# Kernel tuning notes

Measured on AMD Instinct MI355X. Metric: run time of the kernel, lower is better.

Reference implementation:

```python
import jax, jax.numpy as jnp
import numpy as np

B, T, NA, H, C = 64, 128, 2048, 1024, 10  # batch, time, n_act, hidden_units, classes
FORGET_BIAS = 1.0  # tf BasicLSTMCell default


def setup_inputs() -> dict:
    key = jax.random.key(0)
    ks = jax.random.split(key, 5)
    s = 0.02
    return {
        "inputs": jax.random.normal(ks[0], (B, T, NA), jnp.float32),
        "W0": jax.random.normal(ks[1], (NA + H, 4 * H), jnp.float32) * s,
        "b0": jnp.zeros((4 * H,), jnp.float32),
        "W1": jax.random.normal(ks[2], (2 * H, 4 * H), jnp.float32) * s,
        "b1": jnp.zeros((4 * H,), jnp.float32),
        "Wout": jax.random.normal(ks[3], (H, C), jnp.float32) * s,
        "bout": jnp.zeros((C,), jnp.float32),
    }


def _lstm_step(c, h, x, W, b):
    # tf.contrib.rnn.BasicLSTMCell: z = [x; h] @ W + b, gates order i, j, f, o
    z = jnp.concatenate([x, h], axis=-1) @ W + b
    i, j, f, o = jnp.split(z, 4, axis=-1)
    c_new = c * jax.nn.sigmoid(f + FORGET_BIAS) + jax.nn.sigmoid(i) * jnp.tanh(j)
    h_new = jnp.tanh(c_new) * jax.nn.sigmoid(o)
    return c_new, h_new


def reference(inputs, W0, b0, W1, b1, Wout, bout):
    Bz = inputs.shape[0]
    Hd = Wout.shape[0]

    def step(carry, x_t):
        c0, h0, c1, h1 = carry
        c0, h0 = _lstm_step(c0, h0, x_t, W0, b0)   # layer 0
        c1, h1 = _lstm_step(c1, h1, h0, W1, b1)    # layer 1
        return (c0, h0, c1, h1), h1

    z = jnp.zeros((Bz, Hd), inputs.dtype)
    init = (z, z, z, z)  # zero_state for both layers
    xs = jnp.swapaxes(inputs, 0, 1)  # [T, B, NA]
    _, hs = jax.lax.scan(step, init, xs)  # hs: [T, B, H]
    hs = jnp.swapaxes(hs, 0, 1)  # [B, T, H]
    logits = hs @ Wout + bout  # xw_plus_b on flattened outputs
    preds = jax.nn.softmax(logits, axis=-1)  # [B, T, C]
    return preds
```

## Files before the change

### kernel.cpp

```cpp
#include <hip/hip_runtime.h>
#include <stdint.h>


typedef __attribute__((ext_vector_type(4))) float f32x4;
typedef __attribute__((ext_vector_type(8))) short short8x;
typedef unsigned short ushort_t;

constexpr int B_  = 64;
constexpr int T_  = 128;
constexpr int NA_ = 2048;
constexpr int H_  = 1024;
constexpr int C_  = 10;
constexpr int BT_ = B_ * T_;
constexpr int G4_ = 4 * H_;
constexpr int HB_ = B_ * H_;
constexpr int CH_ = 32;
constexpr int MC_ = B_ * CH_;
constexpr int NWG_ = 256;

__device__ __forceinline__ ushort_t f2bf(float x) {
    uint32_t u = __float_as_uint(x);
    uint32_t r = (u + 0x7FFFu + ((u >> 16) & 1u)) >> 16;
    return (ushort_t)r;
}
__device__ __forceinline__ float bf2f(ushort_t h) {
    return __uint_as_float((uint32_t)h << 16);
}
__device__ __forceinline__ float sigmf(float x) { return 1.0f / (1.0f + expf(-x)); }

__device__ __forceinline__ void st_u32(void* p, uint32_t v) {
    __hip_atomic_store((uint32_t*)p, v, __ATOMIC_RELAXED, __HIP_MEMORY_SCOPE_AGENT);
}

#define AH_ISSUE(dst, ptr) \
    asm volatile("global_load_dwordx4 %0, %1, off sc0 sc1" : "=v"(dst) : "v"(ptr))

#define GLOAD_LDS(gp, lp) \
    __builtin_amdgcn_global_load_lds((const __attribute__((address_space(1))) uint32_t*)(gp), \
                                     (__attribute__((address_space(3))) uint32_t*)(lp), 16, 0, 0)

__global__ void decomp_chunk(const float* __restrict__ X, int c,
                             ushort_t* __restrict__ Hi, ushort_t* __restrict__ Lo) {
    const int i = blockIdx.x * blockDim.x + threadIdx.x;
    if (i >= MC_ * NA_ / 4) return;
    const int mp = i >> 9;
    const int kq = i & 511;
    const int b = mp >> 5, j = mp & 31;
    const size_t src = ((size_t)(b * T_ + c * CH_ + j)) * NA_ + (size_t)kq * 4;
    float4 v = *(const float4*)(X + src);
    ushort4 hi, lo;
    hi.x = f2bf(v.x); lo.x = f2bf(v.x - bf2f(hi.x));
    hi.y = f2bf(v.y); lo.y = f2bf(v.y - bf2f(hi.y));
    hi.z = f2bf(v.z); lo.z = f2bf(v.z - bf2f(hi.z));
    hi.w = f2bf(v.w); lo.w = f2bf(v.w - bf2f(hi.w));
    ((ushort4*)Hi)[i] = hi;
    ((ushort4*)Lo)[i] = lo;
}

__global__ void transdec(const float* __restrict__ W, int rowOff, int Klen,
                         ushort_t* __restrict__ Thi, ushort_t* __restrict__ Tlo,
                         int swz) {
    __shared__ float tile[32][33];
    const int k0 = blockIdx.x * 32, n0 = blockIdx.y * 32;
    const int tx = threadIdx.x & 31, ty = threadIdx.x >> 5;
#pragma unroll
    for (int i = 0; i < 32; i += 8)
        tile[ty + i][tx] = W[(size_t)(rowOff + k0 + ty + i) * G4_ + n0 + tx];
    __syncthreads();
#pragma unroll
    for (int i = 0; i < 32; i += 8) {
        float v = tile[tx][ty + i];
        int n = n0 + ty + i;
        int kk = k0 + tx;
        ushort_t hi = f2bf(v);
        Thi[(size_t)n * Klen + kk] = hi;
        int kl = swz ? (kk ^ ((n & 7) << 3)) : kk;
        Tlo[(size_t)n * Klen + kl] = f2bf(v - bf2f(hi));
    }
}

__global__ __launch_bounds__(256, 2)
void gemm_bf16x3(const ushort_t* __restrict__ Ahi, const ushort_t* __restrict__ Alo,
                 const ushort_t* __restrict__ Bhi, const ushort_t* __restrict__ Blo,
                 float* __restrict__ C, int M, int N, int K) {
    __shared__ ushort_t sA[2][128 * 64];
    __shared__ ushort_t sB[2][128 * 64];

    const int tid  = threadIdx.x;
    const int lane = tid & 63;
    const int wv   = tid >> 6;
    const int wr   = wv >> 1, wc = wv & 1;
    const int tiles_n = N >> 7;
    int id = blockIdx.x;
    const int q8 = gridDim.x >> 3;
    id = (id & 7) * q8 + (id >> 3);
    const int tm = (id / tiles_n) * 128, tn = (id % tiles_n) * 128;

    f32x4 acc[4][4] = {};

    for (int k0 = 0; k0 < K; k0 += 64) {
#pragma unroll
        for (int rd = 0; rd < 4; ++rd) {
            const int off = rd * 4096 + tid * 16;
            const int r   = off >> 7;
            const int kc  = ((off >> 4) & 7) ^ (r & 7);
            const size_t aoff = (size_t)(tm + r) * K + k0 + kc * 8;
            const size_t boff = (size_t)(tn + r) * K + k0 + kc * 8;
            const int dst = (rd * 4096 + wv * 1024) >> 1;
            GLOAD_LDS(Ahi + aoff, (ushort_t*)sA[0] + dst);
            GLOAD_LDS(Alo + aoff, (ushort_t*)sA[1] + dst);
            GLOAD_LDS(Bhi + boff, (ushort_t*)sB[0] + dst);
            GLOAD_LDS(Blo + boff, (ushort_t*)sB[1] + dst);
        }
        __syncthreads();
#pragma unroll
        for (int ks = 0; ks < 2; ++ks) {
            short8x ah[4], al[4], bh[4], bl[4];
#pragma unroll
            for (int i = 0; i < 4; ++i) {
                const int kc = ks * 4 + (lane >> 4);
                const int ra = wr * 64 + i * 16 + (lane & 15);
                const int ea = ra * 64 + ((kc ^ (ra & 7)) * 8);
                ah[i] = *(const short8x*)(&sA[0][ea]);
                al[i] = *(const short8x*)(&sA[1][ea]);
                const int rb = wc * 64 + i * 16 + (lane & 15);
                const int eb = rb * 64 + ((kc ^ (rb & 7)) * 8);
                bh[i] = *(const short8x*)(&sB[0][eb]);
                bl[i] = *(const short8x*)(&sB[1][eb]);
            }
#pragma unroll
            for (int i = 0; i < 4; ++i)
#pragma unroll
                for (int j = 0; j < 4; ++j) {
                    acc[i][j] = __builtin_amdgcn_mfma_f32_16x16x32_bf16(ah[i], bh[j], acc[i][j], 0, 0, 0);
                    acc[i][j] = __builtin_amdgcn_mfma_f32_16x16x32_bf16(ah[i], bl[j], acc[i][j], 0, 0, 0);
                    acc[i][j] = __builtin_amdgcn_mfma_f32_16x16x32_bf16(al[i], bh[j], acc[i][j], 0, 0, 0);
                }
        }
        __syncthreads();
    }
#pragma unroll
    for (int i = 0; i < 4; ++i)
#pragma unroll
        for (int j = 0; j < 4; ++j)
#pragma unroll
            for (int qq = 0; qq < 4; ++qq) {
                const int row = tm + wr * 64 + i * 16 + (lane >> 4) * 4 + qq;
                const int col = tn + wc * 64 + j * 16 + (lane & 15);
                C[(size_t)row * N + col] = acc[i][j][qq];
            }
}

__device__ __forceinline__ void grid_bar(unsigned* slots, unsigned* flag, unsigned epoch) {
    __syncthreads();
    if (threadIdx.x == 0)
        __hip_atomic_store(&slots[blockIdx.x], epoch, __ATOMIC_RELAXED, __HIP_MEMORY_SCOPE_AGENT);
    if (blockIdx.x == 0) {
        if (threadIdx.x < NWG_) {
            unsigned spins = 0;
            while (__hip_atomic_load(&slots[threadIdx.x], __ATOMIC_RELAXED, __HIP_MEMORY_SCOPE_AGENT) < epoch
                   && ++spins < (1u << 20))
                __builtin_amdgcn_s_sleep(4);
        }
        __syncthreads();
        if (threadIdx.x == 0)
            __hip_atomic_store(flag, epoch, __ATOMIC_RELAXED, __HIP_MEMORY_SCOPE_AGENT);
    } else {
        if (threadIdx.x == 0) {
            unsigned spins = 0;
            while (__hip_atomic_load(flag, __ATOMIC_RELAXED, __HIP_MEMORY_SCOPE_AGENT) < epoch
                   && ++spins < (1u << 20))
                __builtin_amdgcn_s_sleep(4);
        }
    }
    __syncthreads();
}

__global__ __launch_bounds__(512, 1)
void lstm_persist(int t0, int t1,
                  const float* __restrict__ Z0c,
                  const ushort_t* __restrict__ W0hT_hi, const ushort_t* __restrict__ W0hT_lo,
                  const ushort_t* __restrict__ W1T_hi,  const ushort_t* __restrict__ W1T_lo,
                  const float* __restrict__ b0, const float* __restrict__ b1,
                  ushort_t* __restrict__ h0blk, ushort_t* __restrict__ h1blk,
                  float* __restrict__ c0, float* __restrict__ c1,
                  ushort_t* __restrict__ hsblk, unsigned* slots, unsigned* flag) {
    const int w = blockIdx.x;
    const bool isL0 = (w < 128);
    const int uB = isL0 ? w : (w - 128);
    const int u0 = uB * 8;
    const int tid = threadIdx.x, lane = tid & 63, kv = tid >> 6;
    const int K   = isL0 ? H_ : 2 * H_;
    const int KS  = K >> 3;
    const int NKS = KS >> 5;
    const int kbase = kv * KS;

    __shared__ ushort_t slo[32 * 2048];
    __shared__ float zbuf[64][33];

    const ushort_t* Whi = isL0 ? W0hT_hi : W1T_hi;
    const ushort_t* Wlo = isL0 ? W0hT_lo : W1T_lo;

    const int nis = K >> 9;
    for (int g = 0; g < 4; ++g)
        for (int is = 0; is < nis; ++is) {
            const size_t selem = (size_t)(g * H_ + u0) * K + is * 4096 + kv * 512 + (size_t)lane * 8;
            ushort_t* dst = slo + g * 8 * K + is * 4096 + kv * 512;
            GLOAD_LDS(Wlo + selem, dst);
        }
    short8x wh[2][8] = {};
#pragma unroll
    for (int jn = 0; jn < 2; ++jn)
#pragma unroll
        for (int s = 0; s < 8; ++s)
            if (s < NKS) {
                const int n = jn * 16 + (lane & 15);
                const int grow = (n >> 3) * H_ + u0 + (n & 7);
                wh[jn][s] = *(const short8x*)(Whi + (size_t)grow * K + kbase + s * 32 + (lane >> 4) * 8);
            }
    __syncthreads();

    const bool epi = (tid < 256);
    const int em = tid >> 2;
    const int jp = (tid & 3) * 2;
    const int eu = u0 + jp;
    const float* bias = isL0 ? b0 : b1;
    const float bi0 = epi ? bias[eu]            : 0.f, bi1 = epi ? bias[eu + 1]            : 0.f;
    const float bj0 = epi ? bias[H_ + eu]       : 0.f, bj1 = epi ? bias[H_ + eu + 1]       : 0.f;
    const float bf0 = epi ? bias[2 * H_ + eu]   : 0.f, bf1 = epi ? bias[2 * H_ + eu + 1]   : 0.f;
    const float bo0 = epi ? bias[3 * H_ + eu]   : 0.f, bo1 = epi ? bias[3 * H_ + eu + 1]   : 0.f;
    const int zm = tid >> 3, zj = tid & 7;

    float cr0 = 0.f, cr1 = 0.f;
    float* cptr = (isL0 ? c0 : c1) + (size_t)em * H_ + eu;
    if (epi) { float2 cv = *(const float2*)cptr; cr0 = cv.x; cr1 = cv.y; }

    for (int t = t0; t < t1; ++t) {
        const bool active = isL0 ? (t < T_) : (t >= 1);
        if (active) {
            const int tt = isL0 ? t : t - 1;
            const ushort_t* Ah;
            int ka0;
            if (isL0)          { Ah = h0blk + ((tt + 1) & 1) * HB_; ka0 = kbase; }
            else if (kv < 4)   { Ah = h0blk + (tt & 1) * HB_;       ka0 = kbase; }
            else               { Ah = h1blk + ((tt + 1) & 1) * HB_; ka0 = kbase - H_; }

            zbuf[zm][zj] = 0.f; zbuf[zm][8 + zj] = 0.f;
            zbuf[zm][16 + zj] = 0.f; zbuf[zm][24 + zj] = 0.f;
            __syncthreads();

            float2 zx0 = {0.f, 0.f}, zx1 = {0.f, 0.f}, zx2 = {0.f, 0.f}, zx3 = {0.f, 0.f};
            if (isL0 && epi) {
                const float* zr = Z0c + ((size_t)em * CH_ + (tt & (CH_ - 1))) * G4_;
                zx0 = *(const float2*)(zr + eu);
                zx1 = *(const float2*)(zr + H_ + eu);
                zx2 = *(const float2*)(zr + 2 * H_ + eu);
                zx3 = *(const float2*)(zr + 3 * H_ + eu);
            }

            f32x4 acc[4][2] = {};
            short8x ah[2][4];
            const int npass = NKS >> 1;
#pragma unroll
            for (int pp = 0; pp < 4; ++pp)
                if (pp < npass) {
#pragma unroll
                    for (int s2 = 0; s2 < 2; ++s2) {
                        const int s = pp * 2 + s2;
                        const int kaa = ka0 + s * 32 + (lane >> 4) * 8;
#pragma unroll
                        for (int i = 0; i < 4; ++i) {
                            const int batch = i * 16 + (lane & 15);
                            AH_ISSUE(ah[s2][i], Ah + (size_t)(kaa >> 3) * 512 + (size_t)batch * 8);
                        }
                    }
                    asm volatile("s_waitcnt vmcnt(0)" ::: "memory");
                    __builtin_amdgcn_sched_barrier(0);
#pragma unroll
                    for (int s2 = 0; s2 < 2; ++s2) {
                        const int s = pp * 2 + s2;
                        const int kw = kbase + s * 32 + (lane >> 4) * 8;
                        const int n0_ = (lane & 15);
                        short8x bl0 = *(const short8x*)(&slo[n0_ * K + (kw ^ ((n0_ & 7) << 3))]);
                        const int n1_ = 16 + (lane & 15);
                        short8x bl1 = *(const short8x*)(&slo[n1_ * K + (kw ^ ((n1_ & 7) << 3))]);
#pragma unroll
                        for (int i = 0; i < 4; ++i) {
                            acc[i][0] = __builtin_amdgcn_mfma_f32_16x16x32_bf16(ah[s2][i], wh[0][s], acc[i][0], 0, 0, 0);
                            acc[i][1] = __builtin_amdgcn_mfma_f32_16x16x32_bf16(ah[s2][i], wh[1][s], acc[i][1], 0, 0, 0);
                            acc[i][0] = __builtin_amdgcn_mfma_f32_16x16x32_bf16(ah[s2][i], bl0, acc[i][0], 0, 0, 0);
                            acc[i][1] = __builtin_amdgcn_mfma_f32_16x16x32_bf16(ah[s2][i], bl1, acc[i][1], 0, 0, 0);
                        }
                    }
                }
#pragma unroll
            for (int i2 = 0; i2 < 4; ++i2) {
                const int i = (i2 + (kv & 3)) & 3;
#pragma unroll
                for (int jn2 = 0; jn2 < 2; ++jn2) {
                    const int jn = (jn2 + (kv >> 2)) & 1;
#pragma unroll
                    for (int qq = 0; qq < 4; ++qq) {
                        const int m = i * 16 + (lane >> 4) * 4 + qq;
                        const int n = jn * 16 + (lane & 15);
                        atomicAdd(&zbuf[m][n], acc[i][jn][qq]);
                    }
                }
            }
            __syncthreads();

            if (epi) {
                const float zi0 = zbuf[em][jp]          + bi0 + zx0.x;
                const float zi1 = zbuf[em][jp + 1]      + bi1 + zx0.y;
                const float zj0 = zbuf[em][8 + jp]      + bj0 + zx1.x;
                const float zj1 = zbuf[em][8 + jp + 1]  + bj1 + zx1.y;
                const float zf0 = zbuf[em][16 + jp]     + bf0 + zx2.x;
                const float zf1 = zbuf[em][16 + jp + 1] + bf1 + zx2.y;
                const float zo0 = zbuf[em][24 + jp]     + bo0 + zx3.x;
                const float zo1 = zbuf[em][24 + jp + 1] + bo1 + zx3.y;
                const float cn0 = cr0 * sigmf(zf0 + 1.0f) + sigmf(zi0) * tanhf(zj0);
                const float cn1 = cr1 * sigmf(zf1 + 1.0f) + sigmf(zi1) * tanhf(zj1);
                cr0 = cn0; cr1 = cn1;
                const float hv0 = tanhf(cn0) * sigmf(zo0);
                const float hv1 = tanhf(cn1) * sigmf(zo1);
                const uint32_t hhp = (uint32_t)f2bf(hv0) | ((uint32_t)f2bf(hv1) << 16);
                const size_t hoff = (size_t)uB * 512 + (size_t)em * 8 + jp;
                if (isL0) {
                    st_u32(h0blk + (tt & 1) * HB_ + hoff, hhp);
                } else {
                    st_u32(h1blk + (tt & 1) * HB_ + hoff, hhp);
                    st_u32(hsblk + ((size_t)tt * 128 + uB) * 512 + (size_t)em * 8 + jp, hhp);
                }
            }
        }
        if (t < T_) grid_bar(slots, flag, (unsigned)(t + 1));
    }

    if (epi) { float2 cv; cv.x = cr0; cv.y = cr1; *(float2*)cptr = cv; }
}

__global__ __launch_bounds__(256)
void out_softmax(const ushort_t* __restrict__ hs, const float* __restrict__ Wout,
                 const float* __restrict__ bout, float* __restrict__ out) {
    const int row  = blockIdx.x * 4 + (threadIdx.x >> 6);
    const int lane = threadIdx.x & 63;
    const int b = row >> 7, t = row & (T_ - 1);
    float s[C_];
#pragma unroll
    for (int c = 0; c < C_; ++c) s[c] = 0.f;
    for (int k = lane; k < H_; k += 64) {
        const float hv = bf2f(hs[((size_t)t * 128 + (k >> 3)) * 512 + (size_t)b * 8 + (k & 7)]);
        const float* w = Wout + k * C_;
#pragma unroll
        for (int c = 0; c < C_; ++c) s[c] += hv * w[c];
    }
#pragma unroll
    for (int c = 0; c < C_; ++c) {
#pragma unroll
        for (int d = 32; d > 0; d >>= 1) s[c] += __shfl_xor(s[c], d);
        s[c] += bout[c];
    }
    float mx = s[0];
#pragma unroll
    for (int c = 1; c < C_; ++c) mx = fmaxf(mx, s[c]);
    float sum = 0.f;
#pragma unroll
    for (int c = 0; c < C_; ++c) { s[c] = expf(s[c] - mx); sum += s[c]; }
    const float inv = 1.0f / sum;
    if (lane < C_) {
        float pv = 0.f;
#pragma unroll
        for (int c = 0; c < C_; ++c)
            if (lane == c) pv = s[c] * inv;
        out[(size_t)row * C_ + lane] = pv;
    }
}

extern "C" void kernel_launch(void* const* d_in, const int* in_sizes, int n_in,
                              void* d_out, int out_size, void* d_ws, size_t ws_size,
                              hipStream_t stream) {
    const float* X    = (const float*)d_in[0];
    const float* W0   = (const float*)d_in[1];
    const float* b0   = (const float*)d_in[2];
    const float* W1   = (const float*)d_in[3];
    const float* b1   = (const float*)d_in[4];
    const float* Wout = (const float*)d_in[5];
    const float* bout = (const float*)d_in[6];
    float* out = (float*)d_out;

    char* p = (char*)d_ws;
    size_t off = 0;
    auto take = [&](size_t bytes) { char* r = p + off; off += bytes; return r; };
    ushort_t* W0xT_hi = (ushort_t*)take((size_t)G4_ * NA_ * 2);
    ushort_t* W0xT_lo = (ushort_t*)take((size_t)G4_ * NA_ * 2);
    ushort_t* W0hT_hi = (ushort_t*)take((size_t)G4_ * H_ * 2);
    ushort_t* W0hT_lo = (ushort_t*)take((size_t)G4_ * H_ * 2);
    ushort_t* W1T_hi  = (ushort_t*)take((size_t)G4_ * 2 * H_ * 2);
    ushort_t* W1T_lo  = (ushort_t*)take((size_t)G4_ * 2 * H_ * 2);
    ushort_t* Xc_hi   = (ushort_t*)take((size_t)MC_ * NA_ * 2);
    ushort_t* Xc_lo   = (ushort_t*)take((size_t)MC_ * NA_ * 2);
    float*    Z0c     = (float*)take((size_t)MC_ * G4_ * 4);
    ushort_t* hsblk   = (ushort_t*)take((size_t)BT_ * H_ * 2);
    float*    c0      = (float*)take((size_t)B_ * H_ * 4);
    float*    c1      = (float*)take((size_t)B_ * H_ * 4);
    ushort_t* h0blk   = (ushort_t*)take((size_t)2 * HB_ * 2);
    ushort_t* h1blk   = (ushort_t*)take((size_t)2 * HB_ * 2);
    unsigned* bar     = (unsigned*)take(2048);
    if (ws_size < off) return;

    unsigned* slots = bar;
    unsigned* flag  = bar + 256;

    (void)hipMemsetAsync(c0, 0, (size_t)B_ * H_ * 4, stream);
    (void)hipMemsetAsync(c1, 0, (size_t)B_ * H_ * 4, stream);
    (void)hipMemsetAsync(h0blk + HB_, 0, (size_t)HB_ * 2, stream);
    (void)hipMemsetAsync(h1blk + HB_, 0, (size_t)HB_ * 2, stream);
    (void)hipMemsetAsync(bar, 0, 2048, stream);

    transdec<<<dim3(NA_ / 32, G4_ / 32), 256, 0, stream>>>(W0, 0,   NA_,     W0xT_hi, W0xT_lo, 0);
    transdec<<<dim3(H_  / 32, G4_ / 32), 256, 0, stream>>>(W0, NA_, H_,      W0hT_hi, W0hT_lo, 1);
    transdec<<<dim3(2 * H_ / 32, G4_ / 32), 256, 0, stream>>>(W1, 0, 2 * H_, W1T_hi,  W1T_lo, 1);

    for (int c = 0; c < T_ / CH_; ++c) {
        decomp_chunk<<<(MC_ * NA_ / 4 + 255) / 256, 256, 0, stream>>>(X, c, Xc_hi, Xc_lo);
        gemm_bf16x3<<<(MC_ / 128) * (G4_ / 128), 256, 0, stream>>>(
            Xc_hi, Xc_lo, W0xT_hi, W0xT_lo, Z0c, MC_, G4_, NA_);
        lstm_persist<<<NWG_, 512, 0, stream>>>(c * CH_, c * CH_ + CH_, Z0c,
                                               W0hT_hi, W0hT_lo, W1T_hi, W1T_lo,
                                               b0, b1, h0blk, h1blk,
                                               c0, c1, hsblk, slots, flag);
    }
    lstm_persist<<<NWG_, 512, 0, stream>>>(T_, T_ + 1, Z0c,
                                           W0hT_hi, W0hT_lo, W1T_hi, W1T_lo,
                                           b0, b1, h0blk, h1blk,
                                           c0, c1, hsblk, slots, flag);

    out_softmax<<<BT_ / 4, 256, 0, stream>>>(hsblk, Wout, bout, out);
}
```

Measured before the change: 4.447 ms.

## Drop bf16x3 for recurrent weights and halve persistent LSTM workgroups

The recurrent matmuls now use a single bf16 copy of the weights instead of the hi+lo split, which halves the MFMA count per step. Each workgroup handles 16 hidden units instead of 8 across 128 workgroups, so the grid barrier synchronises half as many blocks. Weights are kept in LDS, with part of W1 held in registers, and the h-state block layout changes to 16-wide to match. This reduces recurrent precision to plain bf16, which risks accuracy drift over 128 timesteps.

Measured after the change: 8.348 ms. 1.88x slower.

```diff
diff --git a/kernel.cpp b/kernel.cpp
--- a/kernel.cpp
+++ b/kernel.cpp
@@ -16,7 +16,7 @@
 constexpr int HB_ = B_ * H_;
 constexpr int CH_ = 32;
 constexpr int MC_ = B_ * CH_;
-constexpr int NWG_ = 256;
+constexpr int NWGP_ = 128;
 
 __device__ __forceinline__ ushort_t f2bf(float x) {
     uint32_t u = __float_as_uint(x);
@@ -58,8 +58,7 @@
 }
 
 __global__ void transdec(const float* __restrict__ W, int rowOff, int Klen,
-                         ushort_t* __restrict__ Thi, ushort_t* __restrict__ Tlo,
-                         int swz) {
+                         ushort_t* __restrict__ Thi, ushort_t* __restrict__ Tlo) {
     __shared__ float tile[32][33];
     const int k0 = blockIdx.x * 32, n0 = blockIdx.y * 32;
     const int tx = threadIdx.x & 31, ty = threadIdx.x >> 5;
@@ -74,8 +73,27 @@
         int kk = k0 + tx;
         ushort_t hi = f2bf(v);
         Thi[(size_t)n * Klen + kk] = hi;
-        int kl = swz ? (kk ^ ((n & 7) << 3)) : kk;
-        Tlo[(size_t)n * Klen + kl] = f2bf(v - bf2f(hi));
+        Tlo[(size_t)n * Klen + kk] = f2bf(v - bf2f(hi));
+    }
+}
+
+__global__ void transdec1(const float* __restrict__ W, int rowOff, int Klen,
+                          ushort_t* __restrict__ Tlin, ushort_t* __restrict__ Tswz) {
+    __shared__ float tile[32][33];
+    const int k0 = blockIdx.x * 32, n0 = blockIdx.y * 32;
+    const int tx = threadIdx.x & 31, ty = threadIdx.x >> 5;
+#pragma unroll
+    for (int i = 0; i < 32; i += 8)
+        tile[ty + i][tx] = W[(size_t)(rowOff + k0 + ty + i) * G4_ + n0 + tx];
+    __syncthreads();
+#pragma unroll
+    for (int i = 0; i < 32; i += 8) {
+        float v = tile[tx][ty + i];
+        int n = n0 + ty + i;
+        int kk = k0 + tx;
+        ushort_t hi = f2bf(v);
+        Tlin[(size_t)n * Klen + kk] = hi;
+        Tswz[(size_t)n * Klen + (kk ^ ((n & 7) << 3))] = hi;
     }
 }
 
@@ -156,7 +174,7 @@
     if (threadIdx.x == 0)
         __hip_atomic_store(&slots[blockIdx.x], epoch, __ATOMIC_RELAXED, __HIP_MEMORY_SCOPE_AGENT);
     if (blockIdx.x == 0) {
-        if (threadIdx.x < NWG_) {
+        if (threadIdx.x < NWGP_) {
             unsigned spins = 0;
             while (__hip_atomic_load(&slots[threadIdx.x], __ATOMIC_RELAXED, __HIP_MEMORY_SCOPE_AGENT) < epoch
                    && ++spins < (1u << 20))
@@ -179,78 +197,71 @@
 __global__ __launch_bounds__(512, 1)
 void lstm_persist(int t0, int t1,
                   const float* __restrict__ Z0c,
-                  const ushort_t* __restrict__ W0hT_hi, const ushort_t* __restrict__ W0hT_lo,
-                  const ushort_t* __restrict__ W1T_hi,  const ushort_t* __restrict__ W1T_lo,
+                  const ushort_t* __restrict__ W0swz,
+                  const ushort_t* __restrict__ W1lin, const ushort_t* __restrict__ W1swz,
                   const float* __restrict__ b0, const float* __restrict__ b1,
                   ushort_t* __restrict__ h0blk, ushort_t* __restrict__ h1blk,
                   float* __restrict__ c0, float* __restrict__ c1,
                   ushort_t* __restrict__ hsblk, unsigned* slots, unsigned* flag) {
     const int w = blockIdx.x;
-    const bool isL0 = (w < 128);
-    const int uB = isL0 ? w : (w - 128);
-    const int u0 = uB * 8;
+    const bool isL0 = (w < 64);
+    const int uB = isL0 ? w : (w - 64);
+    const int u0 = uB * 16;
     const int tid = threadIdx.x, lane = tid & 63, kv = tid >> 6;
-    const int K   = isL0 ? H_ : 2 * H_;
-    const int KS  = K >> 3;
-    const int NKS = KS >> 5;
-    const int kbase = kv * KS;
-
-    __shared__ ushort_t slo[32 * 2048];
-    __shared__ float zbuf[64][33];
-
-    const ushort_t* Whi = isL0 ? W0hT_hi : W1T_hi;
-    const ushort_t* Wlo = isL0 ? W0hT_lo : W1T_lo;
-
-    const int nis = K >> 9;
-    for (int g = 0; g < 4; ++g)
-        for (int is = 0; is < nis; ++is) {
-            const size_t selem = (size_t)(g * H_ + u0) * K + is * 4096 + kv * 512 + (size_t)lane * 8;
-            ushort_t* dst = slo + g * 8 * K + is * 4096 + kv * 512;
-            GLOAD_LDS(Wlo + selem, dst);
-        }
-    short8x wh[2][8] = {};
-#pragma unroll
-    for (int jn = 0; jn < 2; ++jn)
-#pragma unroll
-        for (int s = 0; s < 8; ++s)
-            if (s < NKS) {
-                const int n = jn * 16 + (lane & 15);
-                const int grow = (n >> 3) * H_ + u0 + (n & 7);
-                wh[jn][s] = *(const short8x*)(Whi + (size_t)grow * K + kbase + s * 32 + (lane >> 4) * 8);
-            }
+    const int Klen = isL0 ? H_ : 2 * H_;
+
+    __shared__ ushort_t slo[64 * 1024];
+    __shared__ float zbuf[64][65];
+
+    const ushort_t* Wsw = isL0 ? W0swz : W1swz;
+    for (int r = 0; r < 16; ++r) {
+        const int f   = r * 4096 + tid * 8;
+        const int row = f >> 10;
+        const int kb  = f & 1023;
+        const int grow = (row >> 4) * H_ + u0 + (row & 15);
+        GLOAD_LDS(Wsw + (size_t)grow * Klen + kb, slo + f);
+    }
+    short8x wl[4][4] = {};
+    if (!isL0) {
+#pragma unroll
+        for (int jn = 0; jn < 4; ++jn)
+#pragma unroll
+            for (int s2 = 0; s2 < 4; ++s2) {
+                const int k = kv * 32 + (s2 + 4) * 256 + (lane >> 4) * 8;
+                const int grow = jn * H_ + u0 + (lane & 15);
+                wl[jn][s2] = *(const short8x*)(W1lin + (size_t)grow * 2048 + k);
+            }
+    }
     __syncthreads();
 
-    const bool epi = (tid < 256);
-    const int em = tid >> 2;
-    const int jp = (tid & 3) * 2;
+    const int em = tid >> 3;
+    const int jp = (tid & 7) * 2;
     const int eu = u0 + jp;
     const float* bias = isL0 ? b0 : b1;
-    const float bi0 = epi ? bias[eu]            : 0.f, bi1 = epi ? bias[eu + 1]            : 0.f;
-    const float bj0 = epi ? bias[H_ + eu]       : 0.f, bj1 = epi ? bias[H_ + eu + 1]       : 0.f;
-    const float bf0 = epi ? bias[2 * H_ + eu]   : 0.f, bf1 = epi ? bias[2 * H_ + eu + 1]   : 0.f;
-    const float bo0 = epi ? bias[3 * H_ + eu]   : 0.f, bo1 = epi ? bias[3 * H_ + eu + 1]   : 0.f;
+    const float bi0 = bias[eu],          bi1 = bias[eu + 1];
+    const float bj0 = bias[H_ + eu],     bj1 = bias[H_ + eu + 1];
+    const float bf0 = bias[2 * H_ + eu], bf1 = bias[2 * H_ + eu + 1];
+    const float bo0 = bias[3 * H_ + eu], bo1 = bias[3 * H_ + eu + 1];
     const int zm = tid >> 3, zj = tid & 7;
 
-    float cr0 = 0.f, cr1 = 0.f;
+    float cr0, cr1;
     float* cptr = (isL0 ? c0 : c1) + (size_t)em * H_ + eu;
-    if (epi) { float2 cv = *(const float2*)cptr; cr0 = cv.x; cr1 = cv.y; }
+    { float2 cv = *(const float2*)cptr; cr0 = cv.x; cr1 = cv.y; }
 
     for (int t = t0; t < t1; ++t) {
         const bool active = isL0 ? (t < T_) : (t >= 1);
         if (active) {
             const int tt = isL0 ? t : t - 1;
-            const ushort_t* Ah;
-            int ka0;
-            if (isL0)          { Ah = h0blk + ((tt + 1) & 1) * HB_; ka0 = kbase; }
-            else if (kv < 4)   { Ah = h0blk + (tt & 1) * HB_;       ka0 = kbase; }
-            else               { Ah = h1blk + ((tt + 1) & 1) * HB_; ka0 = kbase - H_; }
-
-            zbuf[zm][zj] = 0.f; zbuf[zm][8 + zj] = 0.f;
-            zbuf[zm][16 + zj] = 0.f; zbuf[zm][24 + zj] = 0.f;
+            const ushort_t* h0prev = h0blk + ((tt + 1) & 1) * HB_;
+            const ushort_t* h0cur  = h0blk + (tt & 1) * HB_;
+            const ushort_t* h1prev = h1blk + ((tt + 1) & 1) * HB_;
+
+#pragma unroll
+            for (int q = 0; q < 8; ++q) zbuf[zm][q * 8 + zj] = 0.f;
             __syncthreads();
 
             float2 zx0 = {0.f, 0.f}, zx1 = {0.f, 0.f}, zx2 = {0.f, 0.f}, zx3 = {0.f, 0.f};
-            if (isL0 && epi) {
+            if (isL0) {
                 const float* zr = Z0c + ((size_t)em * CH_ + (tt & (CH_ - 1))) * G4_;
                 zx0 = *(const float2*)(zr + eu);
                 zx1 = *(const float2*)(zr + H_ + eu);
@@ -258,20 +269,27 @@
                 zx3 = *(const float2*)(zr + 3 * H_ + eu);
             }
 
-            f32x4 acc[4][2] = {};
+            f32x4 acc[4][4] = {};
             short8x ah[2][4];
-            const int npass = NKS >> 1;
+            const int nchunk = isL0 ? 2 : 4;
 #pragma unroll
             for (int pp = 0; pp < 4; ++pp)
-                if (pp < npass) {
+                if (pp < nchunk) {
 #pragma unroll
                     for (int s2 = 0; s2 < 2; ++s2) {
                         const int s = pp * 2 + s2;
-                        const int kaa = ka0 + s * 32 + (lane >> 4) * 8;
+                        const int kg = isL0 ? (kv * 128 + s * 32) : (kv * 32 + s * 256);
+                        const ushort_t* base;
+                        int kk;
+                        if (isL0)           { base = h0prev; kk = kg; }
+                        else if (kg < 1024) { base = h0cur;  kk = kg; }
+                        else                { base = h1prev; kk = kg - 1024; }
+                        const int kaa = kk + (lane >> 4) * 8;
 #pragma unroll
                         for (int i = 0; i < 4; ++i) {
                             const int batch = i * 16 + (lane & 15);
-                            AH_ISSUE(ah[s2][i], Ah + (size_t)(kaa >> 3) * 512 + (size_t)batch * 8);
+                            AH_ISSUE(ah[s2][i],
+                                     base + (size_t)(kaa >> 4) * 1024 + (size_t)batch * 16 + (kaa & 8));
                         }
                     }
                     asm volatile("s_waitcnt vmcnt(0)" ::: "memory");
@@ -279,17 +297,21 @@
 #pragma unroll
                     for (int s2 = 0; s2 < 2; ++s2) {
                         const int s = pp * 2 + s2;
-                        const int kw = kbase + s * 32 + (lane >> 4) * 8;
-                        const int n0_ = (lane & 15);
-                        short8x bl0 = *(const short8x*)(&slo[n0_ * K + (kw ^ ((n0_ & 7) << 3))]);
-                        const int n1_ = 16 + (lane & 15);
-                        short8x bl1 = *(const short8x*)(&slo[n1_ * K + (kw ^ ((n1_ & 7) << 3))]);
-#pragma unroll
-                        for (int i = 0; i < 4; ++i) {
-                            acc[i][0] = __builtin_amdgcn_mfma_f32_16x16x32_bf16(ah[s2][i], wh[0][s], acc[i][0], 0, 0, 0);
-                            acc[i][1] = __builtin_amdgcn_mfma_f32_16x16x32_bf16(ah[s2][i], wh[1][s], acc[i][1], 0, 0, 0);
-                            acc[i][0] = __builtin_amdgcn_mfma_f32_16x16x32_bf16(ah[s2][i], bl0, acc[i][0], 0, 0, 0);
-                            acc[i][1] = __builtin_amdgcn_mfma_f32_16x16x32_bf16(ah[s2][i], bl1, acc[i][1], 0, 0, 0);
+                        const int kg = isL0 ? (kv * 128 + s * 32) : (kv * 32 + s * 256);
+                        const bool useLDS = isL0 || (kg < 1024);
+#pragma unroll
+                        for (int jn = 0; jn < 4; ++jn) {
+                            short8x bw;
+                            if (useLDS) {
+                                const int row  = jn * 16 + (lane & 15);
+                                const int kidx = kg + (lane >> 4) * 8;
+                                bw = *(const short8x*)(&slo[row * 1024 + (kidx ^ ((row & 7) << 3))]);
+                            } else {
+                                bw = wl[jn][s - 4];
+                            }
+#pragma unroll
+                            for (int i = 0; i < 4; ++i)
+                                acc[i][jn] = __builtin_amdgcn_mfma_f32_16x16x32_bf16(ah[s2][i], bw, acc[i][jn], 0, 0, 0);
                         }
                     }
                 }
@@ -297,8 +319,8 @@
             for (int i2 = 0; i2 < 4; ++i2) {
                 const int i = (i2 + (kv & 3)) & 3;
 #pragma unroll
-                for (int jn2 = 0; jn2 < 2; ++jn2) {
-                    const int jn = (jn2 + (kv >> 2)) & 1;
+                for (int jn2 = 0; jn2 < 4; ++jn2) {
+                    const int jn = (jn2 + (kv >> 1)) & 3;
 #pragma unroll
                     for (int qq = 0; qq < 4; ++qq) {
                         const int m = i * 16 + (lane >> 4) * 4 + qq;
@@ -309,34 +331,34 @@
             }
             __syncthreads();
 
-            if (epi) {
+            {
                 const float zi0 = zbuf[em][jp]          + bi0 + zx0.x;
                 const float zi1 = zbuf[em][jp + 1]      + bi1 + zx0.y;
-                const float zj0 = zbuf[em][8 + jp]      + bj0 + zx1.x;
-                const float zj1 = zbuf[em][8 + jp + 1]  + bj1 + zx1.y;
-                const float zf0 = zbuf[em][16 + jp]     + bf0 + zx2.x;
-                const float zf1 = zbuf[em][16 + jp + 1] + bf1 + zx2.y;
-                const float zo0 = zbuf[em][24 + jp]     + bo0 + zx3.x;
-                const float zo1 = zbuf[em][24 + jp + 1] + bo1 + zx3.y;
+                const float zj0 = zbuf[em][16 + jp]     + bj0 + zx1.x;
+                const float zj1 = zbuf[em][16 + jp + 1] + bj1 + zx1.y;
+                const float zf0 = zbuf[em][32 + jp]     + bf0 + zx2.x;
+                const float zf1 = zbuf[em][32 + jp + 1] + bf1 + zx2.y;
+                const float zo0 = zbuf[em][48 + jp]     + bo0 + zx3.x;
+                const float zo1 = zbuf[em][48 + jp + 1] + bo1 + zx3.y;
                 const float cn0 = cr0 * sigmf(zf0 + 1.0f) + sigmf(zi0) * tanhf(zj0);
                 const float cn1 = cr1 * sigmf(zf1 + 1.0f) + sigmf(zi1) * tanhf(zj1);
                 cr0 = cn0; cr1 = cn1;
                 const float hv0 = tanhf(cn0) * sigmf(zo0);
                 const float hv1 = tanhf(cn1) * sigmf(zo1);
                 const uint32_t hhp = (uint32_t)f2bf(hv0) | ((uint32_t)f2bf(hv1) << 16);
-                const size_t hoff = (size_t)uB * 512 + (size_t)em * 8 + jp;
+                const size_t hoff = (size_t)uB * 1024 + (size_t)em * 16 + jp;
                 if (isL0) {
                     st_u32(h0blk + (tt & 1) * HB_ + hoff, hhp);
                 } else {
                     st_u32(h1blk + (tt & 1) * HB_ + hoff, hhp);
-                    st_u32(hsblk + ((size_t)tt * 128 + uB) * 512 + (size_t)em * 8 + jp, hhp);
+                    st_u32(hsblk + (((size_t)tt * 64 + uB) * 64 + em) * 16 + jp, hhp);
                 }
             }
         }
         if (t < T_) grid_bar(slots, flag, (unsigned)(t + 1));
     }
 
-    if (epi) { float2 cv; cv.x = cr0; cv.y = cr1; *(float2*)cptr = cv; }
+    { float2 cv; cv.x = cr0; cv.y = cr1; *(float2*)cptr = cv; }
 }
 
 __global__ __launch_bounds__(256)
@@ -349,7 +371,7 @@
 #pragma unroll
     for (int c = 0; c < C_; ++c) s[c] = 0.f;
     for (int k = lane; k < H_; k += 64) {
-        const float hv = bf2f(hs[((size_t)t * 128 + (k >> 3)) * 512 + (size_t)b * 8 + (k & 7)]);
+        const float hv = bf2f(hs[(((size_t)t * 64 + (k >> 4)) * 64 + b) * 16 + (k & 15)]);
         const float* w = Wout + k * C_;
 #pragma unroll
         for (int c = 0; c < C_; ++c) s[c] += hv * w[c];
@@ -393,10 +415,10 @@
     auto take = [&](size_t bytes) { char* r = p + off; off += bytes; return r; };
     ushort_t* W0xT_hi = (ushort_t*)take((size_t)G4_ * NA_ * 2);
     ushort_t* W0xT_lo = (ushort_t*)take((size_t)G4_ * NA_ * 2);
-    ushort_t* W0hT_hi = (ushort_t*)take((size_t)G4_ * H_ * 2);
-    ushort_t* W0hT_lo = (ushort_t*)take((size_t)G4_ * H_ * 2);
-    ushort_t* W1T_hi  = (ushort_t*)take((size_t)G4_ * 2 * H_ * 2);
-    ushort_t* W1T_lo  = (ushort_t*)take((size_t)G4_ * 2 * H_ * 2);
+    ushort_t* W0h_lin = (ushort_t*)take((size_t)G4_ * H_ * 2);
+    ushort_t* W0h_swz = (ushort_t*)take((size_t)G4_ * H_ * 2);
+    ushort_t* W1_lin  = (ushort_t*)take((size_t)G4_ * 2 * H_ * 2);
+    ushort_t* W1_swz  = (ushort_t*)take((size_t)G4_ * 2 * H_ * 2);
     ushort_t* Xc_hi   = (ushort_t*)take((size_t)MC_ * NA_ * 2);
     ushort_t* Xc_lo   = (ushort_t*)take((size_t)MC_ * NA_ * 2);
     float*    Z0c     = (float*)take((size_t)MC_ * G4_ * 4);
@@ -417,23 +439,23 @@
     (void)hipMemsetAsync(h1blk + HB_, 0, (size_t)HB_ * 2, stream);
     (void)hipMemsetAsync(bar, 0, 2048, stream);
 
-    transdec<<<dim3(NA_ / 32, G4_ / 32), 256, 0, stream>>>(W0, 0,   NA_,     W0xT_hi, W0xT_lo, 0);
-    transdec<<<dim3(H_  / 32, G4_ / 32), 256, 0, stream>>>(W0, NA_, H_,      W0hT_hi, W0hT_lo, 1);
-    transdec<<<dim3(2 * H_ / 32, G4_ / 32), 256, 0, stream>>>(W1, 0, 2 * H_, W1T_hi,  W1T_lo, 1);
+    transdec <<<dim3(NA_ / 32, G4_ / 32), 256, 0, stream>>>(W0, 0, NA_, W0xT_hi, W0xT_lo);
+    transdec1<<<dim3(H_ / 32, G4_ / 32), 256, 0, stream>>>(W0, NA_, H_, W0h_lin, W0h_swz);
+    transdec1<<<dim3(2 * H_ / 32, G4_ / 32), 256, 0, stream>>>(W1, 0, 2 * H_, W1_lin, W1_swz);
 
     for (int c = 0; c < T_ / CH_; ++c) {
         decomp_chunk<<<(MC_ * NA_ / 4 + 255) / 256, 256, 0, stream>>>(X, c, Xc_hi, Xc_lo);
         gemm_bf16x3<<<(MC_ / 128) * (G4_ / 128), 256, 0, stream>>>(
             Xc_hi, Xc_lo, W0xT_hi, W0xT_lo, Z0c, MC_, G4_, NA_);
-        lstm_persist<<<NWG_, 512, 0, stream>>>(c * CH_, c * CH_ + CH_, Z0c,
-                                               W0hT_hi, W0hT_lo, W1T_hi, W1T_lo,
-                                               b0, b1, h0blk, h1blk,
-                                               c0, c1, hsblk, slots, flag);
-    }
-    lstm_persist<<<NWG_, 512, 0, stream>>>(T_, T_ + 1, Z0c,
-                                           W0hT_hi, W0hT_lo, W1T_hi, W1T_lo,
-                                           b0, b1, h0blk, h1blk,
-                                           c0, c1, hsblk, slots, flag);
+        lstm_persist<<<NWGP_, 512, 0, stream>>>(c * CH_, c * CH_ + CH_, Z0c,
+                                                W0h_swz, W1_lin, W1_swz,
+                                                b0, b1, h0blk, h1blk,
+                                                c0, c1, hsblk, slots, flag);
+    }
+    lstm_persist<<<NWGP_, 512, 0, stream>>>(T_, T_ + 1, Z0c,
+                                            W0h_swz, W1_lin, W1_swz,
+                                            b0, b1, h0blk, h1blk,
+                                            c0, c1, hsblk, slots, flag);
 
     out_softmax<<<BT_ / 4, 256, 0, stream>>>(hsblk, Wout, bout, out);
 }
```

## Drop bf16x3 low-part recurrent weights and widen persistent LSTM blocks to 1024 threads

Applied to the files above, without the earlier changes.

The recurrent LSTM kernel now uses only the bf16 high part of the recurrent weights instead of hi+lo split-bf16, which removes the LDS-resident low-weight copy and halves the MFMA count per step. Each block now runs 1024 threads (16 K-slices of 64 lanes), so every wave handles half as many K steps and the per-step serial latency is spread over more waves. The trade-off is a loss of precision in the recurrent matmul, which can accumulate over 128 timesteps and may exceed the tolerance against the fp32 reference. The launch bounds of (1024,4) also look inconsistent with the register-resident weights.

New measurement: 9.127 ms. +105.2%, slower.

```diff
diff --git a/kernel.cpp b/kernel.cpp
--- a/kernel.cpp
+++ b/kernel.cpp
@@ -16,7 +16,7 @@
 constexpr int HB_ = B_ * H_;
 constexpr int CH_ = 32;
 constexpr int MC_ = B_ * CH_;
-constexpr int NWG_ = 256;
+constexpr int NWGP_ = 256;
 
 __device__ __forceinline__ ushort_t f2bf(float x) {
     uint32_t u = __float_as_uint(x);
@@ -58,8 +58,7 @@
 }
 
 __global__ void transdec(const float* __restrict__ W, int rowOff, int Klen,
-                         ushort_t* __restrict__ Thi, ushort_t* __restrict__ Tlo,
-                         int swz) {
+                         ushort_t* __restrict__ Thi, ushort_t* __restrict__ Tlo) {
     __shared__ float tile[32][33];
     const int k0 = blockIdx.x * 32, n0 = blockIdx.y * 32;
     const int tx = threadIdx.x & 31, ty = threadIdx.x >> 5;
@@ -74,8 +73,24 @@
         int kk = k0 + tx;
         ushort_t hi = f2bf(v);
         Thi[(size_t)n * Klen + kk] = hi;
-        int kl = swz ? (kk ^ ((n & 7) << 3)) : kk;
-        Tlo[(size_t)n * Klen + kl] = f2bf(v - bf2f(hi));
+        Tlo[(size_t)n * Klen + kk] = f2bf(v - bf2f(hi));
+    }
+}
+
+__global__ void transb(const float* __restrict__ W, int rowOff, int Klen,
+                       ushort_t* __restrict__ Tq) {
+    __shared__ float tile[32][33];
+    const int k0 = blockIdx.x * 32, n0 = blockIdx.y * 32;
+    const int tx = threadIdx.x & 31, ty = threadIdx.x >> 5;
+#pragma unroll
+    for (int i = 0; i < 32; i += 8)
+        tile[ty + i][tx] = W[(size_t)(rowOff + k0 + ty + i) * G4_ + n0 + tx];
+    __syncthreads();
+#pragma unroll
+    for (int i = 0; i < 32; i += 8) {
+        float v = tile[tx][ty + i];
+        int n = n0 + ty + i;
+        Tq[(size_t)n * Klen + k0 + tx] = f2bf(v);
     }
 }
 
@@ -156,7 +171,7 @@
     if (threadIdx.x == 0)
         __hip_atomic_store(&slots[blockIdx.x], epoch, __ATOMIC_RELAXED, __HIP_MEMORY_SCOPE_AGENT);
     if (blockIdx.x == 0) {
-        if (threadIdx.x < NWG_) {
+        if (threadIdx.x < NWGP_) {
             unsigned spins = 0;
             while (__hip_atomic_load(&slots[threadIdx.x], __ATOMIC_RELAXED, __HIP_MEMORY_SCOPE_AGENT) < epoch
                    && ++spins < (1u << 20))
@@ -176,11 +191,10 @@
     __syncthreads();
 }
 
-__global__ __launch_bounds__(512, 1)
+__global__ __launch_bounds__(1024, 4)
 void lstm_persist(int t0, int t1,
                   const float* __restrict__ Z0c,
-                  const ushort_t* __restrict__ W0hT_hi, const ushort_t* __restrict__ W0hT_lo,
-                  const ushort_t* __restrict__ W1T_hi,  const ushort_t* __restrict__ W1T_lo,
+                  const ushort_t* __restrict__ W0hT, const ushort_t* __restrict__ W1T,
                   const float* __restrict__ b0, const float* __restrict__ b1,
                   ushort_t* __restrict__ h0blk, ushort_t* __restrict__ h1blk,
                   float* __restrict__ c0, float* __restrict__ c1,
@@ -191,34 +205,23 @@
     const int u0 = uB * 8;
     const int tid = threadIdx.x, lane = tid & 63, kv = tid >> 6;
     const int K   = isL0 ? H_ : 2 * H_;
-    const int KS  = K >> 3;
+    const int KS  = K >> 4;
     const int NKS = KS >> 5;
     const int kbase = kv * KS;
 
-    __shared__ ushort_t slo[32 * 2048];
     __shared__ float zbuf[64][33];
 
-    const ushort_t* Whi = isL0 ? W0hT_hi : W1T_hi;
-    const ushort_t* Wlo = isL0 ? W0hT_lo : W1T_lo;
-
-    const int nis = K >> 9;
-    for (int g = 0; g < 4; ++g)
-        for (int is = 0; is < nis; ++is) {
-            const size_t selem = (size_t)(g * H_ + u0) * K + is * 4096 + kv * 512 + (size_t)lane * 8;
-            ushort_t* dst = slo + g * 8 * K + is * 4096 + kv * 512;
-            GLOAD_LDS(Wlo + selem, dst);
-        }
-    short8x wh[2][8] = {};
+    const ushort_t* Whi = isL0 ? W0hT : W1T;
+    short8x wh[2][4] = {};
 #pragma unroll
     for (int jn = 0; jn < 2; ++jn)
 #pragma unroll
-        for (int s = 0; s < 8; ++s)
+        for (int s = 0; s < 4; ++s)
             if (s < NKS) {
                 const int n = jn * 16 + (lane & 15);
                 const int grow = (n >> 3) * H_ + u0 + (n & 7);
                 wh[jn][s] = *(const short8x*)(Whi + (size_t)grow * K + kbase + s * 32 + (lane >> 4) * 8);
             }
-    __syncthreads();
 
     const bool epi = (tid < 256);
     const int em = tid >> 2;
@@ -229,7 +232,7 @@
     const float bj0 = epi ? bias[H_ + eu]       : 0.f, bj1 = epi ? bias[H_ + eu + 1]       : 0.f;
     const float bf0 = epi ? bias[2 * H_ + eu]   : 0.f, bf1 = epi ? bias[2 * H_ + eu + 1]   : 0.f;
     const float bo0 = epi ? bias[3 * H_ + eu]   : 0.f, bo1 = epi ? bias[3 * H_ + eu + 1]   : 0.f;
-    const int zm = tid >> 3, zj = tid & 7;
+    const int zm = tid >> 4, zj = (tid & 15) * 2;
 
     float cr0 = 0.f, cr1 = 0.f;
     float* cptr = (isL0 ? c0 : c1) + (size_t)em * H_ + eu;
@@ -239,14 +242,11 @@
         const bool active = isL0 ? (t < T_) : (t >= 1);
         if (active) {
             const int tt = isL0 ? t : t - 1;
-            const ushort_t* Ah;
-            int ka0;
-            if (isL0)          { Ah = h0blk + ((tt + 1) & 1) * HB_; ka0 = kbase; }
-            else if (kv < 4)   { Ah = h0blk + (tt & 1) * HB_;       ka0 = kbase; }
-            else               { Ah = h1blk + ((tt + 1) & 1) * HB_; ka0 = kbase - H_; }
-
-            zbuf[zm][zj] = 0.f; zbuf[zm][8 + zj] = 0.f;
-            zbuf[zm][16 + zj] = 0.f; zbuf[zm][24 + zj] = 0.f;
+            const ushort_t* h0prev = h0blk + ((tt + 1) & 1) * HB_;
+            const ushort_t* h0cur  = h0blk + (tt & 1) * HB_;
+            const ushort_t* h1prev = h1blk + ((tt + 1) & 1) * HB_;
+
+            zbuf[zm][zj] = 0.f; zbuf[zm][zj + 1] = 0.f;
             __syncthreads();
 
             float2 zx0 = {0.f, 0.f}, zx1 = {0.f, 0.f}, zx2 = {0.f, 0.f}, zx3 = {0.f, 0.f};
@@ -259,38 +259,28 @@
             }
 
             f32x4 acc[4][2] = {};
-            short8x ah[2][4];
-            const int npass = NKS >> 1;
-#pragma unroll
-            for (int pp = 0; pp < 4; ++pp)
-                if (pp < npass) {
-#pragma unroll
-                    for (int s2 = 0; s2 < 2; ++s2) {
-                        const int s = pp * 2 + s2;
-                        const int kaa = ka0 + s * 32 + (lane >> 4) * 8;
-#pragma unroll
-                        for (int i = 0; i < 4; ++i) {
-                            const int batch = i * 16 + (lane & 15);
-                            AH_ISSUE(ah[s2][i], Ah + (size_t)(kaa >> 3) * 512 + (size_t)batch * 8);
-                        }
+            short8x ah[4];
+#pragma unroll
+            for (int s = 0; s < 4; ++s)
+                if (s < NKS) {
+                    const int kg = kbase + s * 32;
+                    const ushort_t* base;
+                    int kk;
+                    if (isL0)           { base = h0prev; kk = kg; }
+                    else if (kg < 1024) { base = h0cur;  kk = kg; }
+                    else                { base = h1prev; kk = kg - 1024; }
+                    const int kaa = kk + (lane >> 4) * 8;
+#pragma unroll
+                    for (int i = 0; i < 4; ++i) {
+                        const int batch = i * 16 + (lane & 15);
+                        AH_ISSUE(ah[i], base + (size_t)(kaa >> 3) * 512 + (size_t)batch * 8);
                     }
                     asm volatile("s_waitcnt vmcnt(0)" ::: "memory");
                     __builtin_amdgcn_sched_barrier(0);
 #pragma unroll
-                    for (int s2 = 0; s2 < 2; ++s2) {
-                        const int s = pp * 2 + s2;
-                        const int kw = kbase + s * 32 + (lane >> 4) * 8;
-                        const int n0_ = (lane & 15);
-                        short8x bl0 = *(const short8x*)(&slo[n0_ * K + (kw ^ ((n0_ & 7) << 3))]);
-                        const int n1_ = 16 + (lane & 15);
-                        short8x bl1 = *(const short8x*)(&slo[n1_ * K + (kw ^ ((n1_ & 7) << 3))]);
-#pragma unroll
-                        for (int i = 0; i < 4; ++i) {
-                            acc[i][0] = __builtin_amdgcn_mfma_f32_16x16x32_bf16(ah[s2][i], wh[0][s], acc[i][0], 0, 0, 0);
-                            acc[i][1] = __builtin_amdgcn_mfma_f32_16x16x32_bf16(ah[s2][i], wh[1][s], acc[i][1], 0, 0, 0);
-                            acc[i][0] = __builtin_amdgcn_mfma_f32_16x16x32_bf16(ah[s2][i], bl0, acc[i][0], 0, 0, 0);
-                            acc[i][1] = __builtin_amdgcn_mfma_f32_16x16x32_bf16(ah[s2][i], bl1, acc[i][1], 0, 0, 0);
-                        }
+                    for (int i = 0; i < 4; ++i) {
+                        acc[i][0] = __builtin_amdgcn_mfma_f32_16x16x32_bf16(ah[i], wh[0][s], acc[i][0], 0, 0, 0);
+                        acc[i][1] = __builtin_amdgcn_mfma_f32_16x16x32_bf16(ah[i], wh[1][s], acc[i][1], 0, 0, 0);
                     }
                 }
 #pragma unroll
@@ -298,7 +288,7 @@
                 const int i = (i2 + (kv & 3)) & 3;
 #pragma unroll
                 for (int jn2 = 0; jn2 < 2; ++jn2) {
-                    const int jn = (jn2 + (kv >> 2)) & 1;
+                    const int jn = (jn2 + ((kv >> 2) & 1)) & 1;
 #pragma unroll
                     for (int qq = 0; qq < 4; ++qq) {
                         const int m = i * 16 + (lane >> 4) * 4 + qq;
@@ -393,10 +383,8 @@
     auto take = [&](size_t bytes) { char* r = p + off; off += bytes; return r; };
     ushort_t* W0xT_hi = (ushort_t*)take((size_t)G4_ * NA_ * 2);
     ushort_t* W0xT_lo = (ushort_t*)take((size_t)G4_ * NA_ * 2);
-    ushort_t* W0hT_hi = (ushort_t*)take((size_t)G4_ * H_ * 2);
-    ushort_t* W0hT_lo = (ushort_t*)take((size_t)G4_ * H_ * 2);
-    ushort_t* W1T_hi  = (ushort_t*)take((size_t)G4_ * 2 * H_ * 2);
-    ushort_t* W1T_lo  = (ushort_t*)take((size_t)G4_ * 2 * H_ * 2);
+    ushort_t* W0hT    = (ushort_t*)take((size_t)G4_ * H_ * 2);
+    ushort_t* W1T     = (ushort_t*)take((size_t)G4_ * 2 * H_ * 2);
     ushort_t* Xc_hi   = (ushort_t*)take((size_t)MC_ * NA_ * 2);
     ushort_t* Xc_lo   = (ushort_t*)take((size_t)MC_ * NA_ * 2);
     float*    Z0c     = (float*)take((size_t)MC_ * G4_ * 4);
@@ -417,23 +405,21 @@
     (void)hipMemsetAsync(h1blk + HB_, 0, (size_t)HB_ * 2, stream);
     (void)hipMemsetAsync(bar, 0, 2048, stream);
 
-    transdec<<<dim3(NA_ / 32, G4_ / 32), 256, 0, stream>>>(W0, 0,   NA_,     W0xT_hi, W0xT_lo, 0);
-    transdec<<<dim3(H_  / 32, G4_ / 32), 256, 0, stream>>>(W0, NA_, H_,      W0hT_hi, W0hT_lo, 1);
-    transdec<<<dim3(2 * H_ / 32, G4_ / 32), 256, 0, stream>>>(W1, 0, 2 * H_, W1T_hi,  W1T_lo, 1);
+    transdec<<<dim3(NA_ / 32, G4_ / 32), 256, 0, stream>>>(W0, 0, NA_, W0xT_hi, W0xT_lo);
+    transb  <<<dim3(H_ / 32, G4_ / 32), 256, 0, stream>>>(W0, NA_, H_, W0hT);
+    transb  <<<dim3(2 * H_ / 32, G4_ / 32), 256, 0, stream>>>(W1, 0, 2 * H_, W1T);
 
     for (int c = 0; c < T_ / CH_; ++c) {
         decomp_chunk<<<(MC_ * NA_ / 4 + 255) / 256, 256, 0, stream>>>(X, c, Xc_hi, Xc_lo);
         gemm_bf16x3<<<(MC_ / 128) * (G4_ / 128), 256, 0, stream>>>(
             Xc_hi, Xc_lo, W0xT_hi, W0xT_lo, Z0c, MC_, G4_, NA_);
-        lstm_persist<<<NWG_, 512, 0, stream>>>(c * CH_, c * CH_ + CH_, Z0c,
-                                               W0hT_hi, W0hT_lo, W1T_hi, W1T_lo,
-                                               b0, b1, h0blk, h1blk,
-                                               c0, c1, hsblk, slots, flag);
-    }
-    lstm_persist<<<NWG_, 512, 0, stream>>>(T_, T_ + 1, Z0c,
-                                           W0hT_hi, W0hT_lo, W1T_hi, W1T_lo,
-                                           b0, b1, h0blk, h1blk,
-                                           c0, c1, hsblk, slots, flag);
+        lstm_persist<<<NWGP_, 1024, 0, stream>>>(c * CH_, c * CH_ + CH_, Z0c,
+                                                 W0hT, W1T, b0, b1, h0blk, h1blk,
+                                                 c0, c1, hsblk, slots, flag);
+    }
+    lstm_persist<<<NWGP_, 1024, 0, stream>>>(T_, T_ + 1, Z0c,
+                                             W0hT, W1T, b0, b1, h0blk, h1blk,
+                                             c0, c1, hsblk, slots, flag);
 
     out_softmax<<<BT_ / 4, 256, 0, stream>>>(hsblk, Wout, bout, out);
 }
```
